# Performance work log

Hardware: AMD Instinct MI355X
Metric: run time of the kernel (lower is better)

Reference implementation:

```python
import jax, jax.numpy as jnp
import numpy as np

L, G, C = 4, 20000, 128
E = 320000
KD = 16
N_ITER = 3
DECAY = 0.5
LN_EPS = 1e-5


def setup_inputs() -> dict:
    key = jax.random.key(0)
    ks = jax.random.split(key, 8)
    x = jax.random.normal(ks[0], (L, G, C), dtype=jnp.float32)
    edge_row = jax.random.randint(ks[1], (E,), 0, G, dtype=jnp.int32)
    edge_col = jax.random.randint(ks[2], (E,), 0, G, dtype=jnp.int32)
    edge_vals = jax.random.uniform(ks[3], (E,), dtype=jnp.float32)
    Wk = jax.random.normal(ks[4], (C, KD), dtype=jnp.float32) / np.sqrt(C)
    Wq = jax.random.normal(ks[5], (C, KD), dtype=jnp.float32) / np.sqrt(C)
    Wv = jax.random.normal(ks[6], (C, C), dtype=jnp.float32) / np.sqrt(C)
    gamma = jnp.ones((C,), dtype=jnp.float32)
    beta = jnp.zeros((C,), dtype=jnp.float32)
    return {"x": x, "edge_row": edge_row, "edge_col": edge_col,
            "edge_vals": edge_vals, "Wk": Wk, "Wq": Wq, "Wv": Wv,
            "gamma": gamma, "beta": beta}


def _spmm(edge_row, edge_col, edge_vals, xm):
    # sparse [G,G] @ dense [G,D] via gather -> scale -> segment_sum
    gathered = xm[edge_col] * edge_vals[:, None]          # [E, D]
    return jax.ops.segment_sum(gathered, edge_row, num_segments=G)


def reference(x, edge_row, edge_col, edge_vals, Wk, Wq, Wv, gamma, beta):
    # x: [L, G, C]
    k = x @ Wk                                            # [L, G, KD]
    q = x @ Wq
    weights = jnp.mean(k * q, axis=-1, keepdims=True)     # [L, G, 1]
    x_acc = x
    # flatten configs into columns: [G, L*C]
    cur = jnp.transpose(x, (1, 0, 2)).reshape(G, L * C)
    for _ in range(1, N_ITER):
        cur = cur * DECAY
        cur = _spmm(edge_row, edge_col, edge_vals, cur)   # [G, L*C]
        xr = jnp.transpose(cur.reshape(G, L, C), (1, 0, 2))  # [L, G, C]
        ck = xr @ Wk
        cq = xr @ Wq
        weights = weights + jnp.mean(ck * cq, axis=-1, keepdims=True)
        x_acc = x_acc + xr
    values = x_acc @ Wv                                   # [L, G, C]
    v = values * weights
    mu = jnp.mean(v, axis=-1, keepdims=True)
    var = jnp.mean(jnp.square(v - mu), axis=-1, keepdims=True)
    out = (v - mu) * jax.lax.rsqrt(var + LN_EPS) * gamma + beta
    return out
```

## Files before the change

### kernel.cpp

```cpp
#include <hip/hip_runtime.h>
#include <hip/hip_bf16.h>

#define L_  4
#define G_  20000
#define C_  128
#define E_  320000
#define KD_ 16
#define LC_ 512
#define DECAY_ 0.5f
#define LN_EPS_ 1e-5f
#define NG_ 16

__device__ __forceinline__ float bflo(unsigned u) { return __uint_as_float(u << 16); }
__device__ __forceinline__ float bfhi(unsigned u) { return __uint_as_float(u & 0xFFFF0000u); }
__device__ __forceinline__ unsigned pack_bf2(float a, float b) {
    __hip_bfloat16 ha = __float2bfloat16(a), hb = __float2bfloat16(b);
    unsigned short ua = *reinterpret_cast<unsigned short*>(&ha);
    unsigned short ub = *reinterpret_cast<unsigned short*>(&hb);
    return (unsigned)ua | ((unsigned)ub << 16);
}

__global__ __launch_bounds__(64) void init_kernel(
        const float* __restrict__ x,
        const float* __restrict__ Wk,
        const float* __restrict__ Wq,
        uint4* __restrict__ cur0,
        float* __restrict__ kq0,
        float* __restrict__ weights) {
    const int g = blockIdx.x;
    const int t = threadIdx.x;
    const int l = t >> 4;
    const int ch = (t & 15) * 8;

    __shared__ float xs[4][132];

    const float4* xr = (const float4*)(x + ((size_t)l * G_ + g) * C_ + ch);
    float4 xa = xr[0], xb = xr[1];
    *(float4*)&xs[l][ch]     = xa;
    *(float4*)&xs[l][ch + 4] = xb;

    uint4 o;
    o.x = pack_bf2(xa.x, xa.y);
    o.y = pack_bf2(xa.z, xa.w);
    o.z = pack_bf2(xb.x, xb.y);
    o.w = pack_bf2(xb.z, xb.w);
    cur0[(size_t)g * 64 + t] = o;
    __syncthreads();

    const int kd = t & 15;
    const float* xrow = xs[l];
    float K = 0.f, Q = 0.f;
#pragma unroll 8
    for (int c = 0; c < C_; ++c) {
        float xv = xrow[c];
        K += xv * Wk[c * KD_ + kd];
        Q += xv * Wq[c * KD_ + kd];
    }
    kq0[(size_t)g * 128 + t]      = K;
    kq0[(size_t)g * 128 + 64 + t] = Q;

    float prod = K * Q;
#pragma unroll
    for (int m = 1; m < 16; m <<= 1) prod += __shfl_xor(prod, m);
    if ((t & 15) == 0) weights[g * 4 + l] = prod * (1.0f / 16.0f);
}

__global__ void hist_kernel(const int* __restrict__ row, int* __restrict__ counts) {
    int e = blockIdx.x * 256 + threadIdx.x;
    if (e < E_) atomicAdd(&counts[row[e]], 1);
}

__global__ __launch_bounds__(256) void scan_blocks_kernel(
        const int* __restrict__ counts, int* __restrict__ offsets,
        int* __restrict__ btot, int n) {
    const int b = blockIdx.x, t = threadIdx.x;
    const int i = b * 256 + t;
    const int lane = t & 63, wid = t >> 6;
    int v = (i < n) ? counts[i] : 0;
    int incl = v;
#pragma unroll
    for (int d = 1; d < 64; d <<= 1) {
        int o = __shfl_up(incl, d);
        if (lane >= d) incl += o;
    }
    __shared__ int ws[4];
    if (lane == 63) ws[wid] = incl;
    __syncthreads();
    int waveoff = 0;
#pragma unroll
    for (int k = 0; k < 4; ++k) if (k < wid) waveoff += ws[k];
    int excl = waveoff + incl - v;
    if (i < n) offsets[i] = excl;
    if (t == 255) btot[b] = waveoff + incl;
}

__global__ __launch_bounds__(128) void scan_totals_kernel(
        int* __restrict__ btot, int* __restrict__ offsets, int n, int nb) {
    const int t = threadIdx.x;
    const int lane = t & 63, wid = t >> 6;
    int v = (t < nb) ? btot[t] : 0;
    int incl = v;
#pragma unroll
    for (int d = 1; d < 64; d <<= 1) {
        int o = __shfl_up(incl, d);
        if (lane >= d) incl += o;
    }
    __shared__ int ws[2];
    if (lane == 63) ws[wid] = incl;
    __syncthreads();
    int off = (wid == 1) ? ws[0] : 0;
    int excl = off + incl - v;
    if (t < nb) btot[t] = excl;
    if (t == nb - 1) offsets[n] = excl + v;
}

__global__ __launch_bounds__(256) void add_base_kernel(
        int* __restrict__ offsets, const int* __restrict__ btot, int n) {
    int i = blockIdx.x * 256 + threadIdx.x;
    if (i < n) offsets[i] += btot[blockIdx.x];
}

__global__ void scatter_kernel(const int* __restrict__ row,
                               const int* __restrict__ col,
                               const float* __restrict__ vals,
                               int* __restrict__ cursor,
                               int* __restrict__ pcol,
                               float* __restrict__ pval) {
    int e = blockIdx.x * 256 + threadIdx.x;
    if (e < E_) {
        int r = row[e];
        int pos = atomicAdd(&cursor[r], 1);
        pcol[pos] = col[e];
        pval[pos] = vals[e] * DECAY_;
    }
}

__global__ __launch_bounds__(64) void spmm_kernel(
        const uint4* __restrict__ cur_in,
        uint4* __restrict__ cur_out,
        const float2* __restrict__ kq_in,
        float2* __restrict__ kq_out,
        const int* __restrict__ offs,
        const int* __restrict__ pcol,
        const float* __restrict__ pval,
        float* __restrict__ weights) {
    const int g = blockIdx.x;
    const int t = threadIdx.x;
    const int s = offs[g], e = offs[g + 1];
    float acc[8];
#pragma unroll
    for (int j = 0; j < 8; ++j) acc[j] = 0.f;
    float2 ka = {0.f, 0.f};
    int i = s;

    for (; i + 4 <= e; i += 4) {
        int   col[4];
        float vv[4];
#pragma unroll
        for (int u = 0; u < 4; ++u) { col[u] = pcol[i + u]; vv[u] = pval[i + u]; }
        uint4  d[4];
        float2 p[4];
#pragma unroll
        for (int u = 0; u < 4; ++u) d[u] = cur_in[(size_t)col[u] * 64 + t];
#pragma unroll
        for (int u = 0; u < 4; ++u) p[u] = kq_in[(size_t)col[u] * 64 + t];
#pragma unroll
        for (int u = 0; u < 4; ++u) {
            acc[0] += vv[u] * bflo(d[u].x); acc[1] += vv[u] * bfhi(d[u].x);
            acc[2] += vv[u] * bflo(d[u].y); acc[3] += vv[u] * bfhi(d[u].y);
            acc[4] += vv[u] * bflo(d[u].z); acc[5] += vv[u] * bfhi(d[u].z);
            acc[6] += vv[u] * bflo(d[u].w); acc[7] += vv[u] * bfhi(d[u].w);
            ka.x   += vv[u] * p[u].x;
            ka.y   += vv[u] * p[u].y;
        }
    }
    for (; i < e; ++i) {
        int c0 = pcol[i];
        float v0 = pval[i];
        uint4 d = cur_in[(size_t)c0 * 64 + t];
        float2 p = kq_in[(size_t)c0 * 64 + t];
        acc[0] += v0 * bflo(d.x); acc[1] += v0 * bfhi(d.x);
        acc[2] += v0 * bflo(d.y); acc[3] += v0 * bfhi(d.y);
        acc[4] += v0 * bflo(d.z); acc[5] += v0 * bfhi(d.z);
        acc[6] += v0 * bflo(d.w); acc[7] += v0 * bfhi(d.w);
        ka.x   += v0 * p.x;
        ka.y   += v0 * p.y;
    }

    uint4 o;
    o.x = pack_bf2(acc[0], acc[1]);
    o.y = pack_bf2(acc[2], acc[3]);
    o.z = pack_bf2(acc[4], acc[5]);
    o.w = pack_bf2(acc[6], acc[7]);
    cur_out[(size_t)g * 64 + t] = o;
    kq_out[(size_t)g * 64 + t] = ka;

    float px = __shfl_xor(ka.x, 32);
    float py = __shfl_xor(ka.y, 32);
    float prod = ka.x * px + ka.y * py;
#pragma unroll
    for (int m = 1; m < 8; m <<= 1) prod += __shfl_xor(prod, m);
    if (t < 32 && (t & 7) == 0) weights[g * 4 + (t >> 3)] += prod * (1.0f / 16.0f);
}

__global__ __launch_bounds__(256) void final_kernel(
        const float* __restrict__ x,
        const uint4* __restrict__ cur1,
        const uint4* __restrict__ cur2,
        const float* __restrict__ weights,
        const float* __restrict__ Wv,
        const float* __restrict__ gamma,
        const float* __restrict__ beta,
        float* __restrict__ out) {
    const int g0 = blockIdx.x * NG_;
    const int t = threadIdx.x;
    __shared__ float a[NG_ * 4][C_];
    __shared__ float wsh[NG_ * 4];

#pragma unroll
    for (int i = 0; i < 4; ++i) {
        int uidx = i * 256 + t;
        int rid  = uidx >> 4;
        int u16  = uidx & 15;
        int gl = rid >> 2, l = rid & 3;
        const float4* xr = (const float4*)(x + ((size_t)l * G_ + (g0 + gl)) * C_ + u16 * 8);
        float4 xa = xr[0], xb = xr[1];
        size_t ci = ((size_t)g0 * 4 + rid) * 16 + u16;
        uint4 c1 = cur1[ci], c2 = cur2[ci];
        float4 s0, s1;
        s0.x = xa.x + bflo(c1.x) + bflo(c2.x);
        s0.y = xa.y + bfhi(c1.x) + bfhi(c2.x);
        s0.z = xa.z + bflo(c1.y) + bflo(c2.y);
        s0.w = xa.w + bfhi(c1.y) + bfhi(c2.y);
        s1.x = xb.x + bflo(c1.z) + bflo(c2.z);
        s1.y = xb.y + bfhi(c1.z) + bfhi(c2.z);
        s1.z = xb.z + bflo(c1.w) + bflo(c2.w);
        s1.w = xb.w + bfhi(c1.w) + bfhi(c2.w);
        float4* ap = (float4*)(&a[rid][u16 * 8]);
        ap[0] = s0;
        ap[1] = s1;
    }
    if (t < NG_ * 4) wsh[t] = weights[g0 * 4 + t];
    __syncthreads();

    const int r = t >> 5;
    const int cg = t & 31;
    float4 acc[8];
#pragma unroll
    for (int j = 0; j < 8; ++j) acc[j] = {0.f, 0.f, 0.f, 0.f};

    for (int c = 0; c < C_; c += 4) {
        float4 wv0 = *(const float4*)(Wv + (size_t)(c + 0) * C_ + cg * 4);
        float4 wv1 = *(const float4*)(Wv + (size_t)(c + 1) * C_ + cg * 4);
        float4 wv2 = *(const float4*)(Wv + (size_t)(c + 2) * C_ + cg * 4);
        float4 wv3 = *(const float4*)(Wv + (size_t)(c + 3) * C_ + cg * 4);
#pragma unroll
        for (int j = 0; j < 8; ++j) {
            float4 av = *(const float4*)(&a[r * 8 + j][c]);
            acc[j].x += av.x * wv0.x + av.y * wv1.x + av.z * wv2.x + av.w * wv3.x;
            acc[j].y += av.x * wv0.y + av.y * wv1.y + av.z * wv2.y + av.w * wv3.y;
            acc[j].z += av.x * wv0.z + av.y * wv1.z + av.z * wv2.z + av.w * wv3.z;
            acc[j].w += av.x * wv0.w + av.y * wv1.w + av.z * wv2.w + av.w * wv3.w;
        }
    }

    float4 gm = *(const float4*)(gamma + cg * 4);
    float4 bt = *(const float4*)(beta + cg * 4);

#pragma unroll
    for (int j = 0; j < 8; ++j) {
        const int rid = r * 8 + j;
        float w = wsh[rid];
        float4 v = {acc[j].x * w, acc[j].y * w, acc[j].z * w, acc[j].w * w};

        float sum = v.x + v.y + v.z + v.w;
#pragma unroll
        for (int m = 1; m < 32; m <<= 1) sum += __shfl_xor(sum, m);
        float mu = sum * (1.0f / 128.0f);
        float4 d = {v.x - mu, v.y - mu, v.z - mu, v.w - mu};
        float ss = d.x * d.x + d.y * d.y + d.z * d.z + d.w * d.w;
#pragma unroll
        for (int m = 1; m < 32; m <<= 1) ss += __shfl_xor(ss, m);
        float rs = rsqrtf(ss * (1.0f / 128.0f) + LN_EPS_);

        float4 o;
        o.x = d.x * rs * gm.x + bt.x;
        o.y = d.y * rs * gm.y + bt.y;
        o.z = d.z * rs * gm.z + bt.z;
        o.w = d.w * rs * gm.w + bt.w;

        const int g_local = rid >> 2;
        const int l = rid & 3;
        *(float4*)(out + ((size_t)l * G_ + (g0 + g_local)) * C_ + cg * 4) = o;
    }
}

extern "C" void kernel_launch(void* const* d_in, const int* in_sizes, int n_in,
                              void* d_out, int out_size, void* d_ws, size_t ws_size,
                              hipStream_t stream) {
    const float* x       = (const float*)d_in[0];
    const int*   e_row   = (const int*)d_in[1];
    const int*   e_col   = (const int*)d_in[2];
    const float* e_val   = (const float*)d_in[3];
    const float* Wk      = (const float*)d_in[4];
    const float* Wq      = (const float*)d_in[5];
    const float* Wv      = (const float*)d_in[6];
    const float* gamma   = (const float*)d_in[7];
    const float* beta    = (const float*)d_in[8];
    float* out = (float*)d_out;

    char* p = (char*)d_ws;
    auto alloc = [&](size_t bytes) -> void* {
        void* r = (void*)p;
        p += (bytes + 255) & ~(size_t)255;
        return r;
    };
    uint4*  cur0    = (uint4*)alloc((size_t)G_ * LC_ * 2);
    uint4*  cur1    = (uint4*)alloc((size_t)G_ * LC_ * 2);
    uint4*  cur2    = (uint4*)alloc((size_t)G_ * LC_ * 2);
    float*  kq0     = (float*)alloc((size_t)G_ * 128 * 4);
    float*  kq1     = (float*)alloc((size_t)G_ * 128 * 4);
    float*  kq2     = (float*)alloc((size_t)G_ * 128 * 4);
    float*  weights = (float*)alloc((size_t)G_ * L_ * 4);
    int*    counts  = (int*)alloc((size_t)G_ * 4);
    int*    offsets = (int*)alloc((size_t)(G_ + 1) * 4);
    int*    cursor  = (int*)alloc((size_t)G_ * 4);
    int*    pcol    = (int*)alloc((size_t)E_ * 4);
    float*  pval    = (float*)alloc((size_t)E_ * 4);
    const int NB    = (G_ + 255) / 256;
    int*    btot    = (int*)alloc((size_t)NB * 4);

    hipMemsetAsync(counts, 0, (size_t)G_ * 4, stream);
    hist_kernel<<<(E_ + 255) / 256, 256, 0, stream>>>(e_row, counts);
    scan_blocks_kernel<<<NB, 256, 0, stream>>>(counts, offsets, btot, G_);
    scan_totals_kernel<<<1, 128, 0, stream>>>(btot, offsets, G_, NB);
    add_base_kernel<<<NB, 256, 0, stream>>>(offsets, btot, G_);
    hipMemcpyAsync(cursor, offsets, (size_t)G_ * 4, hipMemcpyDeviceToDevice, stream);
    scatter_kernel<<<(E_ + 255) / 256, 256, 0, stream>>>(e_row, e_col, e_val,
                                                         cursor, pcol, pval);

    init_kernel<<<G_, 64, 0, stream>>>(x, Wk, Wq, cur0, kq0, weights);

    spmm_kernel<<<G_, 64, 0, stream>>>(cur0, cur1, (const float2*)kq0,
                                       (float2*)kq1, offsets, pcol, pval, weights);
    spmm_kernel<<<G_, 64, 0, stream>>>(cur1, cur2, (const float2*)kq1,
                                       (float2*)kq2, offsets, pcol, pval, weights);

    final_kernel<<<G_ / NG_, 256, 0, stream>>>(x, cur1, cur2, weights, Wv,
                                               gamma, beta, out);
}
```

Baseline: 369.5 us.

## Remap spmm to 8 rows per block, interleave K/Q, pack edges, widen final block

K and Q are stored interleaved as float2 per lane, and column and value are packed into one int2 per edge so each edge needs a single 8-byte nontemporal load. The spmm kernel is reorganised so each 64-thread block covers 8 rows with 8 lanes each over one 64-wide column slice. This spreads each row's gather over 8 blocks and improves locality across neighbouring rows. Weight updates now use atomicAdd because several blocks touch the same row. The final kernel runs 512 threads with 4 rows per thread instead of 8, aiming for more parallelism and fewer registers.

New measurement: 416.3 us. 12.7% more time.

```diff
diff --git a/kernel.cpp b/kernel.cpp
--- a/kernel.cpp
+++ b/kernel.cpp
@@ -25,7 +25,7 @@
         const float* __restrict__ Wk,
         const float* __restrict__ Wq,
         uint4* __restrict__ cur0,
-        float* __restrict__ kq0,
+        float2* __restrict__ kq0,
         float* __restrict__ weights) {
     const int g = blockIdx.x;
     const int t = threadIdx.x;
@@ -56,8 +56,7 @@
         K += xv * Wk[c * KD_ + kd];
         Q += xv * Wq[c * KD_ + kd];
     }
-    kq0[(size_t)g * 128 + t]      = K;
-    kq0[(size_t)g * 128 + 64 + t] = Q;
+    kq0[(size_t)g * 64 + t] = make_float2(K, Q);
 
     float prod = K * Q;
 #pragma unroll
@@ -124,14 +123,12 @@
                                const int* __restrict__ col,
                                const float* __restrict__ vals,
                                int* __restrict__ cursor,
-                               int* __restrict__ pcol,
-                               float* __restrict__ pval) {
+                               int2* __restrict__ edges) {
     int e = blockIdx.x * 256 + threadIdx.x;
     if (e < E_) {
         int r = row[e];
         int pos = atomicAdd(&cursor[r], 1);
-        pcol[pos] = col[e];
-        pval[pos] = vals[e] * DECAY_;
+        edges[pos] = make_int2(col[e], __float_as_int(vals[e] * DECAY_));
     }
 }
 
@@ -141,29 +138,39 @@
         const float2* __restrict__ kq_in,
         float2* __restrict__ kq_out,
         const int* __restrict__ offs,
-        const int* __restrict__ pcol,
-        const float* __restrict__ pval,
+        const int2* __restrict__ edges,
         float* __restrict__ weights) {
-    const int g = blockIdx.x;
+    const int b = blockIdx.x;
+    const int s = b & 7;
+    const int gc = b >> 3;
     const int t = threadIdx.x;
-    const int s = offs[g], e = offs[g + 1];
+    const int grp = t >> 3, ln = t & 7;
+    const int g = gc * 8 + grp;
+    const int slot = s * 8 + ln;
+
+    const int sE = offs[g], eE = offs[g + 1];
     float acc[8];
 #pragma unroll
     for (int j = 0; j < 8; ++j) acc[j] = 0.f;
     float2 ka = {0.f, 0.f};
-    int i = s;
-
-    for (; i + 4 <= e; i += 4) {
-        int   col[4];
+
+    int i = sE;
+    for (; i + 4 <= eE; i += 4) {
+        int   cole[4];
         float vv[4];
 #pragma unroll
-        for (int u = 0; u < 4; ++u) { col[u] = pcol[i + u]; vv[u] = pval[i + u]; }
+        for (int u = 0; u < 4; ++u) {
+            long long e8 = __builtin_nontemporal_load(
+                (const long long*)(edges + i + u));
+            cole[u] = (int)(e8 & 0xffffffffLL);
+            vv[u]   = __int_as_float((int)(e8 >> 32));
+        }
         uint4  d[4];
         float2 p[4];
 #pragma unroll
-        for (int u = 0; u < 4; ++u) d[u] = cur_in[(size_t)col[u] * 64 + t];
-#pragma unroll
-        for (int u = 0; u < 4; ++u) p[u] = kq_in[(size_t)col[u] * 64 + t];
+        for (int u = 0; u < 4; ++u) d[u] = cur_in[(size_t)cole[u] * 64 + slot];
+#pragma unroll
+        for (int u = 0; u < 4; ++u) p[u] = kq_in[(size_t)cole[u] * 64 + slot];
 #pragma unroll
         for (int u = 0; u < 4; ++u) {
             acc[0] += vv[u] * bflo(d[u].x); acc[1] += vv[u] * bfhi(d[u].x);
@@ -174,11 +181,12 @@
             ka.y   += vv[u] * p[u].y;
         }
     }
-    for (; i < e; ++i) {
-        int c0 = pcol[i];
-        float v0 = pval[i];
-        uint4 d = cur_in[(size_t)c0 * 64 + t];
-        float2 p = kq_in[(size_t)c0 * 64 + t];
+    for (; i < eE; ++i) {
+        long long e8 = __builtin_nontemporal_load((const long long*)(edges + i));
+        int c0 = (int)(e8 & 0xffffffffLL);
+        float v0 = __int_as_float((int)(e8 >> 32));
+        uint4 d = cur_in[(size_t)c0 * 64 + slot];
+        float2 p = kq_in[(size_t)c0 * 64 + slot];
         acc[0] += v0 * bflo(d.x); acc[1] += v0 * bfhi(d.x);
         acc[2] += v0 * bflo(d.y); acc[3] += v0 * bfhi(d.y);
         acc[4] += v0 * bflo(d.z); acc[5] += v0 * bfhi(d.z);
@@ -192,18 +200,16 @@
     o.y = pack_bf2(acc[2], acc[3]);
     o.z = pack_bf2(acc[4], acc[5]);
     o.w = pack_bf2(acc[6], acc[7]);
-    cur_out[(size_t)g * 64 + t] = o;
-    kq_out[(size_t)g * 64 + t] = ka;
-
-    float px = __shfl_xor(ka.x, 32);
-    float py = __shfl_xor(ka.y, 32);
-    float prod = ka.x * px + ka.y * py;
+    cur_out[(size_t)g * 64 + slot] = o;
+    kq_out[(size_t)g * 64 + slot] = ka;
+
+    float prod = ka.x * ka.y;
 #pragma unroll
     for (int m = 1; m < 8; m <<= 1) prod += __shfl_xor(prod, m);
-    if (t < 32 && (t & 7) == 0) weights[g * 4 + (t >> 3)] += prod * (1.0f / 16.0f);
-}
-
-__global__ __launch_bounds__(256) void final_kernel(
+    if (ln == 0) atomicAdd(&weights[g * 4 + (s >> 1)], prod * (1.0f / 16.0f));
+}
+
+__global__ __launch_bounds__(512) void final_kernel(
         const float* __restrict__ x,
         const uint4* __restrict__ cur1,
         const uint4* __restrict__ cur2,
@@ -218,8 +224,8 @@
     __shared__ float wsh[NG_ * 4];
 
 #pragma unroll
-    for (int i = 0; i < 4; ++i) {
-        int uidx = i * 256 + t;
+    for (int i = 0; i < 2; ++i) {
+        int uidx = i * 512 + t;
         int rid  = uidx >> 4;
         int u16  = uidx & 15;
         int gl = rid >> 2, l = rid & 3;
@@ -245,9 +251,9 @@
 
     const int r = t >> 5;
     const int cg = t & 31;
-    float4 acc[8];
-#pragma unroll
-    for (int j = 0; j < 8; ++j) acc[j] = {0.f, 0.f, 0.f, 0.f};
+    float4 acc[4];
+#pragma unroll
+    for (int j = 0; j < 4; ++j) acc[j] = {0.f, 0.f, 0.f, 0.f};
 
     for (int c = 0; c < C_; c += 4) {
         float4 wv0 = *(const float4*)(Wv + (size_t)(c + 0) * C_ + cg * 4);
@@ -255,8 +261,8 @@
         float4 wv2 = *(const float4*)(Wv + (size_t)(c + 2) * C_ + cg * 4);
         float4 wv3 = *(const float4*)(Wv + (size_t)(c + 3) * C_ + cg * 4);
 #pragma unroll
-        for (int j = 0; j < 8; ++j) {
-            float4 av = *(const float4*)(&a[r * 8 + j][c]);
+        for (int j = 0; j < 4; ++j) {
+            float4 av = *(const float4*)(&a[r * 4 + j][c]);
             acc[j].x += av.x * wv0.x + av.y * wv1.x + av.z * wv2.x + av.w * wv3.x;
             acc[j].y += av.x * wv0.y + av.y * wv1.y + av.z * wv2.y + av.w * wv3.y;
             acc[j].z += av.x * wv0.z + av.y * wv1.z + av.z * wv2.z + av.w * wv3.z;
@@ -268,8 +274,8 @@
     float4 bt = *(const float4*)(beta + cg * 4);
 
 #pragma unroll
-    for (int j = 0; j < 8; ++j) {
-        const int rid = r * 8 + j;
+    for (int j = 0; j < 4; ++j) {
+        const int rid = r * 4 + j;
         float w = wsh[rid];
         float4 v = {acc[j].x * w, acc[j].y * w, acc[j].z * w, acc[j].w * w};
 
@@ -318,15 +324,14 @@
     uint4*  cur0    = (uint4*)alloc((size_t)G_ * LC_ * 2);
     uint4*  cur1    = (uint4*)alloc((size_t)G_ * LC_ * 2);
     uint4*  cur2    = (uint4*)alloc((size_t)G_ * LC_ * 2);
-    float*  kq0     = (float*)alloc((size_t)G_ * 128 * 4);
-    float*  kq1     = (float*)alloc((size_t)G_ * 128 * 4);
-    float*  kq2     = (float*)alloc((size_t)G_ * 128 * 4);
+    float2* kq0     = (float2*)alloc((size_t)G_ * 64 * 8);
+    float2* kq1     = (float2*)alloc((size_t)G_ * 64 * 8);
+    float2* kq2     = (float2*)alloc((size_t)G_ * 64 * 8);
     float*  weights = (float*)alloc((size_t)G_ * L_ * 4);
     int*    counts  = (int*)alloc((size_t)G_ * 4);
     int*    offsets = (int*)alloc((size_t)(G_ + 1) * 4);
     int*    cursor  = (int*)alloc((size_t)G_ * 4);
-    int*    pcol    = (int*)alloc((size_t)E_ * 4);
-    float*  pval    = (float*)alloc((size_t)E_ * 4);
+    int2*   edges   = (int2*)alloc((size_t)E_ * 8);
     const int NB    = (G_ + 255) / 256;
     int*    btot    = (int*)alloc((size_t)NB * 4);
 
@@ -337,15 +342,15 @@
     add_base_kernel<<<NB, 256, 0, stream>>>(offsets, btot, G_);
     hipMemcpyAsync(cursor, offsets, (size_t)G_ * 4, hipMemcpyDeviceToDevice, stream);
     scatter_kernel<<<(E_ + 255) / 256, 256, 0, stream>>>(e_row, e_col, e_val,
-                                                         cursor, pcol, pval);
+                                                         cursor, edges);
 
     init_kernel<<<G_, 64, 0, stream>>>(x, Wk, Wq, cur0, kq0, weights);
 
-    spmm_kernel<<<G_, 64, 0, stream>>>(cur0, cur1, (const float2*)kq0,
-                                       (float2*)kq1, offsets, pcol, pval, weights);
-    spmm_kernel<<<G_, 64, 0, stream>>>(cur1, cur2, (const float2*)kq1,
-                                       (float2*)kq2, offsets, pcol, pval, weights);
-
-    final_kernel<<<G_ / NG_, 256, 0, stream>>>(x, cur1, cur2, weights, Wv,
+    spmm_kernel<<<G_, 64, 0, stream>>>(cur0, cur1, kq0, kq1,
+                                       offsets, edges, weights);
+    spmm_kernel<<<G_, 64, 0, stream>>>(cur1, cur2, kq1, kq2,
+                                       offsets, edges, weights);
+
+    final_kernel<<<G_ / NG_, 512, 0, stream>>>(x, cur1, cur2, weights, Wv,
                                                gamma, beta, out);
 }
```
